# Optimization experiments

Hardware: AMD Instinct MI355X
Metric: run time of the kernel (lower is better)

## Reference

```python
import jax, jax.numpy as jnp
import numpy as np

DIM = 1024
NUM_HEAD = 16
DIM_HEAD = DIM // NUM_HEAD
MAX_SEQ_LEN = 4096
RMS_EPS = 1.1920928955078125e-07  # torch nn.RMSNorm default eps = finfo(fp32).eps
LIN_EPS = 1e-6
PAD_VAL = 1.0
THETA = 10000.0


def rmsnorm(x, g):
    return x * jax.lax.rsqrt(jnp.mean(x * x, axis=-1, keepdims=True) + RMS_EPS) * g


def setup_inputs() -> dict:
    key = jax.random.key(0)
    ks = jax.random.split(key, 20)
    B, L, C, D = 4, 2048, 256, DIM
    s = 1.0 / np.sqrt(D)
    inp = {
        "x": jax.random.normal(ks[0], (B, L, D), jnp.float32),
        "context": jax.random.normal(ks[1], (B, C, D), jnp.float32),
        "attn_mask": jax.random.randint(ks[2], (B, L, L), 0, 2).astype(bool),
        "start_pos": jax.random.randint(ks[3], (B,), 0, MAX_SEQ_LEN - L).astype(jnp.int64),
        "Wqkv": jax.random.normal(ks[4], (D, 3 * D), jnp.float32) * s,
        "bqkv": jax.random.normal(ks[5], (3 * D,), jnp.float32) * 0.01,
        "g_q": jnp.ones((D,), jnp.float32),
        "g_k": jnp.ones((D,), jnp.float32),
        "cWqkv": jax.random.normal(ks[6], (D, 3 * D), jnp.float32) * s,
        "cbqkv": jax.random.normal(ks[7], (3 * D,), jnp.float32) * 0.01,
        "cg_q": jnp.ones((D,), jnp.float32),
        "cg_k": jnp.ones((D,), jnp.float32),
        "Wout": jax.random.normal(ks[8], (D, D), jnp.float32) * s,
        "bout": jax.random.normal(ks[9], (D,), jnp.float32) * 0.01,
        "g_out": jnp.ones((D,), jnp.float32),
        "cWout": jax.random.normal(ks[10], (D, D), jnp.float32) * s,
        "cbout": jax.random.normal(ks[11], (D,), jnp.float32) * 0.01,
        "cg_out": jnp.ones((D,), jnp.float32),
    }
    return inp


def _freqs(pos_indices):
    # pos_indices: (B, L) int
    inv = 1.0 / (THETA ** (jnp.arange(0, DIM_HEAD, 2, dtype=jnp.float32) / DIM_HEAD))  # (DH/2,)
    ang = pos_indices.astype(jnp.float32)[..., None] * inv  # (B, L, DH/2)
    return jnp.cos(ang), jnp.sin(ang)


def _apply_rope(t, cos, sin):
    # t: (B, H, L, DH); cos/sin: (B, L, DH/2) -> broadcast over head
    B, H, L, DH = t.shape
    tr = t.reshape(B, H, L, DH // 2, 2)
    t0, t1 = tr[..., 0], tr[..., 1]
    c = cos[:, None]  # (B,1,L,DH/2)
    s = sin[:, None]
    out = jnp.stack([t0 * c - t1 * s, t0 * s + t1 * c], axis=-1)
    return out.reshape(B, H, L, DH)


def _split_heads(t):
    B, L, D = t.shape
    return t.reshape(B, L, NUM_HEAD, DIM_HEAD).transpose(0, 2, 1, 3)


def _augment_mask(m, C):
    # m: (B, L, L) bool -> (B, L+C, L+C) bool
    B, L, _ = m.shape
    c_to_seq = jnp.broadcast_to(jnp.any(m, axis=1, keepdims=True), (B, C, L))
    seq_to_c = jnp.broadcast_to(jnp.any(m, axis=2, keepdims=True), (B, L, C))
    c_to_c = jnp.ones((B, C, C), bool)
    top = jnp.concatenate([m, seq_to_c], axis=2)
    bot = jnp.concatenate([c_to_seq, c_to_c], axis=2)
    return jnp.concatenate([top, bot], axis=1)


def reference(x, context, attn_mask, start_pos, Wqkv, bqkv, g_q, g_k,
              cWqkv, cbqkv, cg_q, cg_k, Wout, bout, g_out, cWout, cbout, cg_out):
    B, L, D = x.shape
    C = context.shape[1]

    q, k, v = jnp.split(x @ Wqkv + bqkv, 3, axis=-1)
    q = rmsnorm(q, g_q)
    k = rmsnorm(k, g_k)
    q, k, v = _split_heads(q), _split_heads(k), _split_heads(v)  # (B,H,L,DH)

    pos = start_pos[:, None] + jnp.arange(L, dtype=start_pos.dtype)[None]  # (B,L)
    cos, sin = _freqs(pos)
    q = _apply_rope(q, cos, sin)
    k = _apply_rope(k, cos, sin)

    cq, ck, cv = jnp.split(context @ cWqkv + cbqkv, 3, axis=-1)
    cq = rmsnorm(cq, cg_q)
    ck = rmsnorm(ck, cg_k)
    cq, ck, cv = _split_heads(cq), _split_heads(ck), _split_heads(cv)

    q = jnp.concatenate([q, cq], axis=2)  # (B,H,S,DH), S=L+C
    k = jnp.concatenate([k, ck], axis=2)
    v = jnp.concatenate([v, cv], axis=2)

    full_mask = _augment_mask(attn_mask, C)[:, None]  # (B,1,S,S)

    # linear attention: ReLU feature map + padded-value trick
    qf = jax.nn.relu(q)
    kf = jax.nn.relu(k)
    k_mask = full_mask[:, :, 0, :][..., None].astype(kf.dtype)  # (B,1,S,1)
    kf = kf * k_mask
    vpad = jnp.pad(v, ((0, 0), (0, 0), (0, 0), (0, 1)), constant_values=PAD_VAL)  # (B,H,S,DH+1)
    vk = jnp.einsum('bhse,bhsd->bhed', vpad, kf)        # (B,H,DH+1,DH)
    res = jnp.einsum('bhed,bhqd->bhqe', vk, qf)          # (B,H,S,DH+1)
    attn = res[..., :-1] / (res[..., -1:] + LIN_EPS)     # (B,H,S,DH)

    attn = attn.transpose(0, 2, 1, 3).reshape(B, L + C, D)
    x_out = rmsnorm(attn[:, :L] @ Wout + bout, g_out)
    c_out = rmsnorm(attn[:, L:] @ cWout + cbout, cg_out)
    return x_out, c_out
```

## Files before the change

kernel.cpp:

```cpp
#include <hip/hip_runtime.h>

typedef __bf16 bf16;
typedef __bf16 bf16x4 __attribute__((ext_vector_type(4)));
typedef __bf16 bf16x8 __attribute__((ext_vector_type(8)));
typedef float  floatx4 __attribute__((ext_vector_type(4)));

#define L_SEQ   2048
#define C_SEQ   256
#define S_SEQ   2304
#define NBATCH  4
#define NHEAD   16
#define DHEAD   64
#define DMODEL  1024
#define RMS_EPS 1.1920928955078125e-07f
#define LIN_EPS 1e-6f

__device__ __forceinline__ void gload_lds16(const void* g, void* l) {
  __builtin_amdgcn_global_load_lds(
      (const __attribute__((address_space(1))) void*)g,
      (__attribute__((address_space(3))) void*)l, 16, 0, 0);
}

__global__ __launch_bounds__(256) void transpose_f32_bf16(
    const float* __restrict__ src, bf16* __restrict__ dst, int R, int C) {
  __shared__ bf16 tile[32][33];
  int c0 = blockIdx.x * 32, r0 = blockIdx.y * 32;
  int tx = threadIdx.x & 31, ty = threadIdx.x >> 5;
  for (int i = ty; i < 32; i += 8)
    tile[i][tx] = (bf16)src[(size_t)(r0 + i) * C + c0 + tx];
  __syncthreads();
  for (int i = ty; i < 32; i += 8)
    dst[(size_t)(c0 + i) * R + r0 + tx] = tile[tx][i];
}

__global__ __launch_bounds__(256) void convert_bf16(
    const float* __restrict__ src, bf16* __restrict__ dst, size_t n) {
  size_t i = ((size_t)blockIdx.x * 256 + threadIdx.x) * 8;
  if (i >= n) return;
  floatx4 a = *(const floatx4*)(src + i);
  floatx4 b = *(const floatx4*)(src + i + 4);
  bf16x8 o;
#pragma unroll
  for (int j = 0; j < 4; j++) { o[j] = (bf16)a[j]; o[4 + j] = (bf16)b[j]; }
  *(bf16x8*)(dst + i) = o;
}

template <bool SCATTER>
__global__ __launch_bounds__(256) void gemm_bias(
    const bf16* __restrict__ A, const bf16* __restrict__ Bt,
    const float* __restrict__ bias, bf16* __restrict__ C0,
    bf16* __restrict__ qs, bf16* __restrict__ ks, bf16* __restrict__ vs,
    int M, int N, int K, int rpb_shift, int seq_off) {
  __shared__ bf16 As[128 * 32];
  __shared__ bf16 Bs[128 * 32];
  int n0 = blockIdx.x * 128, m0 = blockIdx.y * 128;
  int t = threadIdx.x;
  int lane = t & 63, w = t >> 6;
  int wm = (w & 1) * 64, wn = (w >> 1) * 64;
  int l16 = lane & 15, l4 = lane >> 4;

  int srow = w * 32 + (lane >> 2);
  int scol = (lane & 3) * 8;
  const bf16* Ab = A  + (size_t)(m0 + srow) * K + scol;
  const bf16* Bb = Bt + (size_t)(n0 + srow) * K + scol;

  floatx4 acc[4][4] = {};
  for (int kb = 0; kb < K; kb += 32) {
    __syncthreads();
#pragma unroll
    for (int j = 0; j < 2; j++) {
      gload_lds16(Ab + (size_t)j * 16 * K + kb, (char*)As + (w * 2 + j) * 1024);
      gload_lds16(Bb + (size_t)j * 16 * K + kb, (char*)Bs + (w * 2 + j) * 1024);
    }
    __syncthreads();
    bf16x8 af[4], bfr[4];
#pragma unroll
    for (int i = 0; i < 4; i++) {
      af[i]  = *(const bf16x8*)&As[(wm + i * 16 + l16) * 32 + l4 * 8];
      bfr[i] = *(const bf16x8*)&Bs[(wn + i * 16 + l16) * 32 + l4 * 8];
    }
#pragma unroll
    for (int i = 0; i < 4; i++)
#pragma unroll
      for (int j = 0; j < 4; j++)
        acc[i][j] = __builtin_amdgcn_mfma_f32_16x16x32_bf16(af[i], bfr[j], acc[i][j], 0, 0, 0);
  }
#pragma unroll
  for (int i = 0; i < 4; i++)
#pragma unroll
    for (int j = 0; j < 4; j++) {
      int col = n0 + wn + j * 16 + l16;
      float bval = bias[col];
      if constexpr (SCATTER) {
        int which = col >> 10;
        int h = (col >> 6) & 15;
        int dh = col & 63;
        int rmask = (1 << rpb_shift) - 1;
        if (which == 2) {
          int rw0 = m0 + wm + i * 16 + l4 * 4;
          int b = rw0 >> rpb_shift;
          int s = seq_off + (rw0 & rmask);
          bf16x4 o;
#pragma unroll
          for (int r = 0; r < 4; r++) o[r] = (bf16)(acc[i][j][r] + bval);
          *(bf16x4*)(vs + ((size_t)(b * NHEAD + h) * DHEAD + dh) * S_SEQ + s) = o;
        } else {
          bf16* dst = which == 0 ? qs : ks;
#pragma unroll
          for (int r = 0; r < 4; r++) {
            int rw = m0 + wm + i * 16 + l4 * 4 + r;
            int b = rw >> rpb_shift;
            int s = seq_off + (rw & rmask);
            dst[((size_t)(b * NHEAD + h) * S_SEQ + s) * DHEAD + dh] =
                (bf16)(acc[i][j][r] + bval);
          }
        }
      } else {
#pragma unroll
        for (int r = 0; r < 4; r++) {
          int rw = m0 + wm + i * 16 + l4 * 4 + r;
          C0[(size_t)rw * N + col] = (bf16)(acc[i][j][r] + bval);
        }
      }
    }
}

__global__ __launch_bounds__(256) void anymask_kernel(
    const int* __restrict__ mask, int* __restrict__ anym) {
  int b = blockIdx.x, t = threadIdx.x;
  int a = 0;
  size_t base = (size_t)b * L_SEQ * L_SEQ;
  for (int j = t; j < L_SEQ; j += 256) a |= mask[base + j];
  __shared__ int sh;
  if (t == 0) sh = 0;
  __syncthreads();
  if (a) atomicOr(&sh, 1);
  __syncthreads();
  if (t == 0) anym[b] = sh;
}

__global__ __launch_bounds__(256) void zero_f32(float* __restrict__ p, int n) {
  for (int i = blockIdx.x * 256 + threadIdx.x; i < n; i += gridDim.x * 256)
    p[i] = 0.f;
}

__global__ __launch_bounds__(256) void qkv_post(
    bf16* __restrict__ qs, bf16* __restrict__ ks,
    const int* __restrict__ mask, const int* __restrict__ spos,
    const int* __restrict__ anym,
    const float* __restrict__ g_q, const float* __restrict__ g_k,
    const float* __restrict__ cg_q, const float* __restrict__ cg_k) {
  int g = blockIdx.x, t = threadIdx.x;
  bool is_ctx = g >= NBATCH * L_SEQ;
  int b, s;
  const float *gq, *gk;
  float mval;
  if (!is_ctx) {
    b = g >> 11;
    int l = g & 2047;
    s = l;
    mval = mask[(size_t)b * L_SEQ * L_SEQ + l] ? 1.f : 0.f;
    gq = g_q; gk = g_k;
  } else {
    int gg = g - NBATCH * L_SEQ;
    b = gg >> 8;
    s = L_SEQ + (gg & 255);
    mval = anym[b] ? 1.f : 0.f;
    gq = cg_q; gk = cg_k;
  }
  int d0 = t * 4;
  int h = t >> 4, dh = (t & 15) * 4;
  size_t base = ((size_t)(b * NHEAD + h) * S_SEQ + s) * DHEAD + dh;
  bf16x4 q4 = *(const bf16x4*)(qs + base);
  bf16x4 k4 = *(const bf16x4*)(ks + base);
  float qv[4], kv[4], pq = 0.f, pk = 0.f;
#pragma unroll
  for (int i = 0; i < 4; i++) {
    qv[i] = (float)q4[i]; kv[i] = (float)k4[i];
    pq += qv[i] * qv[i];  pk += kv[i] * kv[i];
  }
  int lane = t & 63, w = t >> 6;
  for (int off = 32; off > 0; off >>= 1) {
    pq += __shfl_down(pq, off, 64);
    pk += __shfl_down(pk, off, 64);
  }
  __shared__ float red[8];
  if (lane == 0) { red[w] = pq; red[4 + w] = pk; }
  __syncthreads();
  float sq = red[0] + red[1] + red[2] + red[3];
  float sk = red[4] + red[5] + red[6] + red[7];
  float scq = rsqrtf(sq * (1.f / DMODEL) + RMS_EPS);
  float sck = rsqrtf(sk * (1.f / DMODEL) + RMS_EPS);
#pragma unroll
  for (int i = 0; i < 4; i++) {
    qv[i] *= scq * gq[d0 + i];
    kv[i] *= sck * gk[d0 + i];
  }
  if (!is_ctx) {
    float p = (float)(spos[b] + s);
#pragma unroll
    for (int pr = 0; pr < 2; pr++) {
      int fi = (dh >> 1) + pr;
      float ang = p * expf((float)fi * -0.28782313662425572f);
      float cc = cosf(ang), ss = sinf(ang);
      float t0 = qv[2 * pr], t1 = qv[2 * pr + 1];
      qv[2 * pr]     = t0 * cc - t1 * ss;
      qv[2 * pr + 1] = t0 * ss + t1 * cc;
      t0 = kv[2 * pr]; t1 = kv[2 * pr + 1];
      kv[2 * pr]     = t0 * cc - t1 * ss;
      kv[2 * pr + 1] = t0 * ss + t1 * cc;
    }
  }
  bf16x4 qo, ko;
#pragma unroll
  for (int i = 0; i < 4; i++) {
    qo[i] = (bf16)fmaxf(qv[i], 0.f);
    ko[i] = (bf16)(fmaxf(kv[i], 0.f) * mval);
  }
  *(bf16x4*)(qs + base) = qo;
  *(bf16x4*)(ks + base) = ko;
}

#define VK_CH   8
#define VK_SPAN (S_SEQ / VK_CH)
__global__ __launch_bounds__(256) void vk_mfma(
    const bf16* __restrict__ vT, const bf16* __restrict__ kf,
    float* __restrict__ vk) {
  __shared__ bf16 Vs[64][40];
  __shared__ bf16 Ks[64][40];
  int bh = blockIdx.x >> 3, chunk = blockIdx.x & 7;
  int t = threadIdx.x, lane = t & 63, w = t >> 6;
  int l16 = lane & 15, l4 = lane >> 4;
  const bf16* vp = vT + (size_t)bh * DHEAD * S_SEQ;
  const bf16* kp = kf + (size_t)bh * S_SEQ * DHEAD;
  int s_begin = chunk * VK_SPAN;
  int ve = t >> 2, vso = (t & 3) * 8;
  int ks_s = t & 31, kd0 = (t >> 5) * 8;
  floatx4 acc[4] = {};
  float dsum[8] = {};
  for (int st = 0; st < VK_SPAN; st += 32) {
    int s0 = s_begin + st;
    bf16x8 vv = *(const bf16x8*)(vp + (size_t)ve * S_SEQ + s0 + vso);
    bf16x8 kv = *(const bf16x8*)(kp + (size_t)(s0 + ks_s) * DHEAD + kd0);
    __syncthreads();
    *(bf16x8*)&Vs[ve][vso] = vv;
#pragma unroll
    for (int j = 0; j < 8; j++) {
      Ks[kd0 + j][ks_s] = kv[j];
      dsum[j] += (float)kv[j];
    }
    __syncthreads();
    bf16x8 af = *(const bf16x8*)&Vs[w * 16 + l16][l4 * 8];
#pragma unroll
    for (int nt = 0; nt < 4; nt++) {
      bf16x8 bfr = *(const bf16x8*)&Ks[nt * 16 + l16][l4 * 8];
      acc[nt] = __builtin_amdgcn_mfma_f32_16x16x32_bf16(af, bfr, acc[nt], 0, 0, 0);
    }
  }
  float* vkbh = vk + (size_t)bh * 65 * 64;
#pragma unroll
  for (int nt = 0; nt < 4; nt++)
#pragma unroll
    for (int r = 0; r < 4; r++)
      atomicAdd(&vkbh[(w * 16 + l4 * 4 + r) * 64 + nt * 16 + l16], acc[nt][r]);
#pragma unroll
  for (int j = 0; j < 8; j++)
#pragma unroll
    for (int off = 16; off > 0; off >>= 1)
      dsum[j] += __shfl_down(dsum[j], off, 32);
  if ((lane & 31) == 0)
#pragma unroll
    for (int j = 0; j < 8; j++)
      atomicAdd(&vkbh[64 * 64 + kd0 + j], dsum[j]);
}

__global__ __launch_bounds__(256) void res_attn(
    const bf16* __restrict__ qf, const float* __restrict__ vk,
    bf16* __restrict__ attn_x, bf16* __restrict__ attn_c) {
  __shared__ bf16 Bs[80][72];
  __shared__ float sden[256];
  int bh = blockIdx.x / 9, mblk = blockIdx.x % 9;
  int b = bh >> 4, h = bh & 15;
  int t = threadIdx.x, lane = t & 63, w = t >> 6;
  const float* vkp = vk + (size_t)bh * 65 * 64;
  for (int i = t; i < 80 * 64; i += 256) {
    int e = i >> 6, d = i & 63;
    Bs[e][d] = (bf16)(e < 65 ? vkp[i] : 0.f);
  }
  __syncthreads();
  int l16 = lane & 15, l4 = lane >> 4;
  const bf16* qbase = qf + (size_t)bh * S_SEQ * DHEAD;
  int q0w = mblk * 256 + w * 64;

  floatx4 acc[4][5] = {};
  bf16x8 af[4][2], bfr[5][2];
#pragma unroll
  for (int mt = 0; mt < 4; mt++) {
    int q = q0w + mt * 16 + l16;
    af[mt][0] = *(const bf16x8*)(qbase + (size_t)q * 64 + l4 * 8);
    af[mt][1] = *(const bf16x8*)(qbase + (size_t)q * 64 + 32 + l4 * 8);
  }
#pragma unroll
  for (int nt = 0; nt < 5; nt++) {
    bfr[nt][0] = *(const bf16x8*)&Bs[nt * 16 + l16][l4 * 8];
    bfr[nt][1] = *(const bf16x8*)&Bs[nt * 16 + l16][32 + l4 * 8];
  }
#pragma unroll
  for (int mt = 0; mt < 4; mt++)
#pragma unroll
    for (int nt = 0; nt < 5; nt++) {
      acc[mt][nt] = __builtin_amdgcn_mfma_f32_16x16x32_bf16(af[mt][0], bfr[nt][0], acc[mt][nt], 0, 0, 0);
      acc[mt][nt] = __builtin_amdgcn_mfma_f32_16x16x32_bf16(af[mt][1], bfr[nt][1], acc[mt][nt], 0, 0, 0);
    }
  if (l16 == 0) {
#pragma unroll
    for (int mt = 0; mt < 4; mt++)
#pragma unroll
      for (int r = 0; r < 4; r++)
        sden[w * 64 + mt * 16 + l4 * 4 + r] = acc[mt][4][r];
  }
  __syncthreads();
#pragma unroll
  for (int mt = 0; mt < 4; mt++)
#pragma unroll
    for (int r = 0; r < 4; r++) {
      float den = sden[w * 64 + mt * 16 + l4 * 4 + r] + LIN_EPS;
      float rden = 1.f / den;
      int q = q0w + mt * 16 + l4 * 4 + r;
#pragma unroll
      for (int nt = 0; nt < 4; nt++) {
        int dcol = nt * 16 + l16;
        float a = acc[mt][nt][r] * rden;
        if (q < L_SEQ)
          attn_x[((size_t)b * L_SEQ + q) * DMODEL + h * DHEAD + dcol] = (bf16)a;
        else
          attn_c[((size_t)b * C_SEQ + (q - L_SEQ)) * DMODEL + h * DHEAD + dcol] = (bf16)a;
      }
    }
}

__global__ __launch_bounds__(256) void final_norm(
    const bf16* __restrict__ y_x, const bf16* __restrict__ y_c,
    const float* __restrict__ g_out, const float* __restrict__ cg_out,
    float* __restrict__ out) {
  int g = blockIdx.x, t = threadIdx.x;
  const bf16* src;
  const float* gv;
  if (g < NBATCH * L_SEQ) {
    src = y_x + (size_t)g * DMODEL; gv = g_out;
  } else {
    int gg = g - NBATCH * L_SEQ;
    src = y_c + (size_t)gg * DMODEL; gv = cg_out;
  }
  float* dst = out + (size_t)g * DMODEL;
  int d0 = t * 4;
  bf16x4 y4 = *(const bf16x4*)(src + d0);
  float yv[4], p = 0.f;
#pragma unroll
  for (int i = 0; i < 4; i++) { yv[i] = (float)y4[i]; p += yv[i] * yv[i]; }
  int lane = t & 63, w = t >> 6;
  for (int off = 32; off > 0; off >>= 1) p += __shfl_down(p, off, 64);
  __shared__ float red[4];
  if (lane == 0) red[w] = p;
  __syncthreads();
  float ssum = red[0] + red[1] + red[2] + red[3];
  float sc = rsqrtf(ssum * (1.f / DMODEL) + RMS_EPS);
  floatx4 o;
#pragma unroll
  for (int i = 0; i < 4; i++) o[i] = yv[i] * sc * gv[d0 + i];
  *(floatx4*)(dst + d0) = o;
}

extern "C" void kernel_launch(void* const* d_in, const int* in_sizes, int n_in,
                              void* d_out, int out_size, void* d_ws, size_t ws_size,
                              hipStream_t stream) {
  const float* x      = (const float*)d_in[0];
  const float* ctx    = (const float*)d_in[1];
  const int*   mask   = (const int*)d_in[2];
  const int*   spos   = (const int*)d_in[3];
  const float* Wqkv   = (const float*)d_in[4];
  const float* bqkv   = (const float*)d_in[5];
  const float* g_q    = (const float*)d_in[6];
  const float* g_k    = (const float*)d_in[7];
  const float* cWqkv  = (const float*)d_in[8];
  const float* cbqkv  = (const float*)d_in[9];
  const float* cg_q   = (const float*)d_in[10];
  const float* cg_k   = (const float*)d_in[11];
  const float* Wout   = (const float*)d_in[12];
  const float* bout   = (const float*)d_in[13];
  const float* g_out  = (const float*)d_in[14];
  const float* cWout  = (const float*)d_in[15];
  const float* cbout  = (const float*)d_in[16];
  const float* cg_out = (const float*)d_in[17];

  char* wsp = (char*)d_ws;
  size_t off = 0;
  auto alloc = [&](size_t bytes) -> void* {
    void* p = wsp + off;
    off += (bytes + 255) & ~(size_t)255;
    return p;
  };
  bf16* WqkvT  = (bf16*)alloc((size_t)3072 * 1024 * 2);
  bf16* cWqkvT = (bf16*)alloc((size_t)3072 * 1024 * 2);
  bf16* WoutT  = (bf16*)alloc((size_t)1024 * 1024 * 2);
  bf16* cWoutT = (bf16*)alloc((size_t)1024 * 1024 * 2);
  bf16* xbf    = (bf16*)alloc((size_t)NBATCH * L_SEQ * DMODEL * 2);
  bf16* cbf    = (bf16*)alloc((size_t)NBATCH * C_SEQ * DMODEL * 2);
  const size_t SLAB = (size_t)NBATCH * NHEAD * S_SEQ * DHEAD;
  bf16* qfs    = (bf16*)alloc(SLAB * 2);
  bf16* kfs    = (bf16*)alloc(SLAB * 2);
  bf16* vfs    = (bf16*)alloc(SLAB * 2);
  float* vkw   = (float*)alloc((size_t)64 * 65 * 64 * 4);
  int* anym    = (int*)alloc(256);
  bf16* attn_x = kfs;
  bf16* attn_c = kfs + (size_t)NBATCH * L_SEQ * DMODEL;
  bf16* y_x    = vfs;
  bf16* y_c    = vfs + (size_t)NBATCH * L_SEQ * DMODEL;

  transpose_f32_bf16<<<dim3(96, 32), 256, 0, stream>>>(Wqkv, WqkvT, 1024, 3072);
  transpose_f32_bf16<<<dim3(96, 32), 256, 0, stream>>>(cWqkv, cWqkvT, 1024, 3072);
  transpose_f32_bf16<<<dim3(32, 32), 256, 0, stream>>>(Wout, WoutT, 1024, 1024);
  transpose_f32_bf16<<<dim3(32, 32), 256, 0, stream>>>(cWout, cWoutT, 1024, 1024);
  convert_bf16<<<4096, 256, 0, stream>>>(x, xbf, (size_t)NBATCH * L_SEQ * DMODEL);
  convert_bf16<<<512, 256, 0, stream>>>(ctx, cbf, (size_t)NBATCH * C_SEQ * DMODEL);

  gemm_bias<true><<<dim3(24, 64), 256, 0, stream>>>(
      xbf, WqkvT, bqkv, nullptr, qfs, kfs, vfs, 8192, 3072, 1024, 11, 0);
  gemm_bias<true><<<dim3(24, 8), 256, 0, stream>>>(
      cbf, cWqkvT, cbqkv, nullptr, qfs, kfs, vfs, 1024, 3072, 1024, 8, L_SEQ);

  anymask_kernel<<<4, 256, 0, stream>>>(mask, anym);
  zero_f32<<<1040, 256, 0, stream>>>(vkw, 64 * 65 * 64);

  qkv_post<<<NBATCH * (L_SEQ + C_SEQ), 256, 0, stream>>>(
      qfs, kfs, mask, spos, anym, g_q, g_k, cg_q, cg_k);

  vk_mfma<<<64 * VK_CH, 256, 0, stream>>>(vfs, kfs, vkw);

  res_attn<<<576, 256, 0, stream>>>(qfs, vkw, attn_x, attn_c);

  gemm_bias<false><<<dim3(8, 64), 256, 0, stream>>>(
      attn_x, WoutT, bout, y_x, nullptr, nullptr, nullptr, 8192, 1024, 1024, 0, 0);
  gemm_bias<false><<<dim3(8, 8), 256, 0, stream>>>(
      attn_c, cWoutT, cbout, y_c, nullptr, nullptr, nullptr, 1024, 1024, 1024, 0, 0);

  final_norm<<<NBATCH * (L_SEQ + C_SEQ), 256, 0, stream>>>(
      y_x, y_c, g_out, cg_out, (float*)d_out);
}
```

Before: 410.8 us.

## Fuse prep kernels, merge paired GEMMs, double-buffer GEMM and vk LDS tiles

The transpose, convert, zero and any-mask kernels are merged into one prep launch, and the x and context GEMMs are each combined into a single grouped launch with XCD-aware workgroup remapping. The GEMM main loop now double-buffers its LDS tiles, issuing the next global-to-LDS load before the MFMAs on the current tile, which removes one barrier per iteration. vk_mfma also double-buffers its shared tiles and prefetches the next chunk into registers. The goals are fewer launches, better tail utilisation and overlap of memory with compute, at the cost of twice the LDS per block.

```diff
diff --git a/kernel.cpp b/kernel.cpp
--- a/kernel.cpp
+++ b/kernel.cpp
@@ -21,10 +21,11 @@
       (__attribute__((address_space(3))) void*)l, 16, 0, 0);
 }
 
-__global__ __launch_bounds__(256) void transpose_f32_bf16(
-    const float* __restrict__ src, bf16* __restrict__ dst, int R, int C) {
-  __shared__ bf16 tile[32][33];
-  int c0 = blockIdx.x * 32, r0 = blockIdx.y * 32;
+__device__ __forceinline__ void transpose_job(
+    const float* __restrict__ src, bf16* __restrict__ dst,
+    int R, int C, int tb, bf16 (*tile)[33]) {
+  int tilesx = C >> 5;
+  int c0 = (tb % tilesx) * 32, r0 = (tb / tilesx) * 32;
   int tx = threadIdx.x & 31, ty = threadIdx.x >> 5;
   for (int i = ty; i < 32; i += 8)
     tile[i][tx] = (bf16)src[(size_t)(r0 + i) * C + c0 + tx];
@@ -33,10 +34,9 @@
     dst[(size_t)(c0 + i) * R + r0 + tx] = tile[tx][i];
 }
 
-__global__ __launch_bounds__(256) void convert_bf16(
-    const float* __restrict__ src, bf16* __restrict__ dst, size_t n) {
-  size_t i = ((size_t)blockIdx.x * 256 + threadIdx.x) * 8;
-  if (i >= n) return;
+__device__ __forceinline__ void convert_job(
+    const float* __restrict__ src, bf16* __restrict__ dst, int tb) {
+  size_t i = ((size_t)tb * 256 + threadIdx.x) * 8;
   floatx4 a = *(const floatx4*)(src + i);
   floatx4 b = *(const floatx4*)(src + i + 4);
   bf16x8 o;
@@ -45,15 +45,78 @@
   *(bf16x8*)(dst + i) = o;
 }
 
+__global__ __launch_bounds__(256) void prep(
+    const float* __restrict__ Wqkv, const float* __restrict__ cWqkv,
+    const float* __restrict__ Wout, const float* __restrict__ cWout,
+    const float* __restrict__ x, const float* __restrict__ ctx,
+    const int* __restrict__ mask,
+    bf16* __restrict__ WqkvT, bf16* __restrict__ cWqkvT,
+    bf16* __restrict__ WoutT, bf16* __restrict__ cWoutT,
+    bf16* __restrict__ xbf, bf16* __restrict__ cbf,
+    float* __restrict__ vkw, int* __restrict__ anym) {
+  __shared__ bf16 tile[32][33];
+  __shared__ int sh;
+  int b = blockIdx.x;
+  if (b < 3072) { transpose_job(Wqkv, WqkvT, 1024, 3072, b, tile); return; }
+  b -= 3072;
+  if (b < 3072) { transpose_job(cWqkv, cWqkvT, 1024, 3072, b, tile); return; }
+  b -= 3072;
+  if (b < 1024) { transpose_job(Wout, WoutT, 1024, 1024, b, tile); return; }
+  b -= 1024;
+  if (b < 1024) { transpose_job(cWout, cWoutT, 1024, 1024, b, tile); return; }
+  b -= 1024;
+  if (b < 4096) { convert_job(x, xbf, b); return; }
+  b -= 4096;
+  if (b < 512) { convert_job(ctx, cbf, b); return; }
+  b -= 512;
+  if (b < 260) {
+    int i = b * 1024 + threadIdx.x * 4;
+    *(floatx4*)(vkw + i) = floatx4{0.f, 0.f, 0.f, 0.f};
+    return;
+  }
+  b -= 260;
+  int a = 0;
+  size_t base = (size_t)b * L_SEQ * L_SEQ;
+  for (int j = threadIdx.x; j < L_SEQ; j += 256) a |= mask[base + j];
+  if (threadIdx.x == 0) sh = 0;
+  __syncthreads();
+  if (a) atomicOr(&sh, 1);
+  __syncthreads();
+  if (threadIdx.x == 0) anym[b] = sh;
+}
+
 template <bool SCATTER>
 __global__ __launch_bounds__(256) void gemm_bias(
-    const bf16* __restrict__ A, const bf16* __restrict__ Bt,
-    const float* __restrict__ bias, bf16* __restrict__ C0,
+    const bf16* __restrict__ A1, const bf16* __restrict__ A2,
+    const bf16* __restrict__ B1t, const bf16* __restrict__ B2t,
+    const float* __restrict__ bias1, const float* __restrict__ bias2,
+    bf16* __restrict__ C1, bf16* __restrict__ C2,
     bf16* __restrict__ qs, bf16* __restrict__ ks, bf16* __restrict__ vs,
-    int M, int N, int K, int rpb_shift, int seq_off) {
-  __shared__ bf16 As[128 * 32];
-  __shared__ bf16 Bs[128 * 32];
-  int n0 = blockIdx.x * 128, m0 = blockIdx.y * 128;
+    int N, int K, int ybound,
+    int rpb1, int soff1, int rpb2, int soff2) {
+  __shared__ bf16 As[2][4096];
+  __shared__ bf16 Bs[2][4096];
+
+  int nwg = gridDim.x * gridDim.y;
+  int wg = blockIdx.y * gridDim.x + blockIdx.x;
+  if ((nwg & 7) == 0) {
+    int cpx = nwg >> 3;
+    wg = (wg & 7) * cpx + (wg >> 3);
+  }
+  int bx = wg % gridDim.x, by = wg / gridDim.x;
+  int n0 = bx * 128;
+  const bf16 *Ap, *Bt;
+  const float* bias;
+  bf16* Cp;
+  int m0, rpb, soff;
+  if (by < ybound) {
+    Ap = A1; Bt = B1t; bias = bias1; Cp = C1;
+    m0 = by * 128; rpb = rpb1; soff = soff1;
+  } else {
+    Ap = A2; Bt = B2t; bias = bias2; Cp = C2;
+    m0 = (by - ybound) * 128; rpb = rpb2; soff = soff2;
+  }
+
   int t = threadIdx.x;
   int lane = t & 63, w = t >> 6;
   int wm = (w & 1) * 64, wn = (w >> 1) * 64;
@@ -61,29 +124,36 @@
 
   int srow = w * 32 + (lane >> 2);
   int scol = (lane & 3) * 8;
-  const bf16* Ab = A  + (size_t)(m0 + srow) * K + scol;
+  const bf16* Ab = Ap + (size_t)(m0 + srow) * K + scol;
   const bf16* Bb = Bt + (size_t)(n0 + srow) * K + scol;
 
+  auto stage = [&](int buf, int kb) {
+#pragma unroll
+    for (int j = 0; j < 2; j++) {
+      gload_lds16(Ab + (size_t)j * 16 * K + kb, (char*)&As[buf][(w * 2 + j) * 512]);
+      gload_lds16(Bb + (size_t)j * 16 * K + kb, (char*)&Bs[buf][(w * 2 + j) * 512]);
+    }
+  };
+
   floatx4 acc[4][4] = {};
+  stage(0, 0);
+  __syncthreads();
+  int cur = 0;
   for (int kb = 0; kb < K; kb += 32) {
-    __syncthreads();
-#pragma unroll
-    for (int j = 0; j < 2; j++) {
-      gload_lds16(Ab + (size_t)j * 16 * K + kb, (char*)As + (w * 2 + j) * 1024);
-      gload_lds16(Bb + (size_t)j * 16 * K + kb, (char*)Bs + (w * 2 + j) * 1024);
-    }
-    __syncthreads();
+    if (kb + 32 < K) stage(cur ^ 1, kb + 32);
     bf16x8 af[4], bfr[4];
 #pragma unroll
     for (int i = 0; i < 4; i++) {
-      af[i]  = *(const bf16x8*)&As[(wm + i * 16 + l16) * 32 + l4 * 8];
-      bfr[i] = *(const bf16x8*)&Bs[(wn + i * 16 + l16) * 32 + l4 * 8];
+      af[i]  = *(const bf16x8*)&As[cur][(wm + i * 16 + l16) * 32 + l4 * 8];
+      bfr[i] = *(const bf16x8*)&Bs[cur][(wn + i * 16 + l16) * 32 + l4 * 8];
     }
 #pragma unroll
     for (int i = 0; i < 4; i++)
 #pragma unroll
       for (int j = 0; j < 4; j++)
         acc[i][j] = __builtin_amdgcn_mfma_f32_16x16x32_bf16(af[i], bfr[j], acc[i][j], 0, 0, 0);
+    __syncthreads();
+    cur ^= 1;
   }
 #pragma unroll
   for (int i = 0; i < 4; i++)
@@ -95,11 +165,11 @@
         int which = col >> 10;
         int h = (col >> 6) & 15;
         int dh = col & 63;
-        int rmask = (1 << rpb_shift) - 1;
+        int rmask = (1 << rpb) - 1;
         if (which == 2) {
           int rw0 = m0 + wm + i * 16 + l4 * 4;
-          int b = rw0 >> rpb_shift;
-          int s = seq_off + (rw0 & rmask);
+          int b = rw0 >> rpb;
+          int s = soff + (rw0 & rmask);
           bf16x4 o;
 #pragma unroll
           for (int r = 0; r < 4; r++) o[r] = (bf16)(acc[i][j][r] + bval);
@@ -109,8 +179,8 @@
 #pragma unroll
           for (int r = 0; r < 4; r++) {
             int rw = m0 + wm + i * 16 + l4 * 4 + r;
-            int b = rw >> rpb_shift;
-            int s = seq_off + (rw & rmask);
+            int b = rw >> rpb;
+            int s = soff + (rw & rmask);
             dst[((size_t)(b * NHEAD + h) * S_SEQ + s) * DHEAD + dh] =
                 (bf16)(acc[i][j][r] + bval);
           }
@@ -119,29 +189,10 @@
 #pragma unroll
         for (int r = 0; r < 4; r++) {
           int rw = m0 + wm + i * 16 + l4 * 4 + r;
-          C0[(size_t)rw * N + col] = (bf16)(acc[i][j][r] + bval);
+          Cp[(size_t)rw * N + col] = (bf16)(acc[i][j][r] + bval);
         }
       }
     }
-}
-
-__global__ __launch_bounds__(256) void anymask_kernel(
-    const int* __restrict__ mask, int* __restrict__ anym) {
-  int b = blockIdx.x, t = threadIdx.x;
-  int a = 0;
-  size_t base = (size_t)b * L_SEQ * L_SEQ;
-  for (int j = t; j < L_SEQ; j += 256) a |= mask[base + j];
-  __shared__ int sh;
-  if (t == 0) sh = 0;
-  __syncthreads();
-  if (a) atomicOr(&sh, 1);
-  __syncthreads();
-  if (t == 0) anym[b] = sh;
-}
-
-__global__ __launch_bounds__(256) void zero_f32(float* __restrict__ p, int n) {
-  for (int i = blockIdx.x * 256 + threadIdx.x; i < n; i += gridDim.x * 256)
-    p[i] = 0.f;
 }
 
 __global__ __launch_bounds__(256) void qkv_post(
@@ -226,8 +277,8 @@
 __global__ __launch_bounds__(256) void vk_mfma(
     const bf16* __restrict__ vT, const bf16* __restrict__ kf,
     float* __restrict__ vk) {
-  __shared__ bf16 Vs[64][40];
-  __shared__ bf16 Ks[64][40];
+  __shared__ bf16 Vs[2][64][40];
+  __shared__ bf16 Ks[2][64][40];
   int bh = blockIdx.x >> 3, chunk = blockIdx.x & 7;
   int t = threadIdx.x, lane = t & 63, w = t >> 6;
   int l16 = lane & 15, l4 = lane >> 4;
@@ -238,22 +289,26 @@
   int ks_s = t & 31, kd0 = (t >> 5) * 8;
   floatx4 acc[4] = {};
   float dsum[8] = {};
+  bf16x8 vv = *(const bf16x8*)(vp + (size_t)ve * S_SEQ + s_begin + vso);
+  bf16x8 kv = *(const bf16x8*)(kp + (size_t)(s_begin + ks_s) * DHEAD + kd0);
   for (int st = 0; st < VK_SPAN; st += 32) {
-    int s0 = s_begin + st;
-    bf16x8 vv = *(const bf16x8*)(vp + (size_t)ve * S_SEQ + s0 + vso);
-    bf16x8 kv = *(const bf16x8*)(kp + (size_t)(s0 + ks_s) * DHEAD + kd0);
+    int cur = (st >> 5) & 1;
+    *(bf16x8*)&Vs[cur][ve][vso] = vv;
+#pragma unroll
+    for (int j = 0; j < 8; j++) {
+      Ks[cur][kd0 + j][ks_s] = kv[j];
+      dsum[j] += (float)kv[j];
+    }
+    if (st + 32 < VK_SPAN) {
+      int s0 = s_begin + st + 32;
+      vv = *(const bf16x8*)(vp + (size_t)ve * S_SEQ + s0 + vso);
+      kv = *(const bf16x8*)(kp + (size_t)(s0 + ks_s) * DHEAD + kd0);
+    }
     __syncthreads();
-    *(bf16x8*)&Vs[ve][vso] = vv;
-#pragma unroll
-    for (int j = 0; j < 8; j++) {
-      Ks[kd0 + j][ks_s] = kv[j];
-      dsum[j] += (float)kv[j];
-    }
-    __syncthreads();
-    bf16x8 af = *(const bf16x8*)&Vs[w * 16 + l16][l4 * 8];
+    bf16x8 af = *(const bf16x8*)&Vs[cur][w * 16 + l16][l4 * 8];
 #pragma unroll
     for (int nt = 0; nt < 4; nt++) {
-      bf16x8 bfr = *(const bf16x8*)&Ks[nt * 16 + l16][l4 * 8];
+      bf16x8 bfr = *(const bf16x8*)&Ks[cur][nt * 16 + l16][l4 * 8];
       acc[nt] = __builtin_amdgcn_mfma_f32_16x16x32_bf16(af, bfr, acc[nt], 0, 0, 0);
     }
   }
@@ -417,20 +472,13 @@
   bf16* y_x    = vfs;
   bf16* y_c    = vfs + (size_t)NBATCH * L_SEQ * DMODEL;
 
-  transpose_f32_bf16<<<dim3(96, 32), 256, 0, stream>>>(Wqkv, WqkvT, 1024, 3072);
-  transpose_f32_bf16<<<dim3(96, 32), 256, 0, stream>>>(cWqkv, cWqkvT, 1024, 3072);
-  transpose_f32_bf16<<<dim3(32, 32), 256, 0, stream>>>(Wout, WoutT, 1024, 1024);
-  transpose_f32_bf16<<<dim3(32, 32), 256, 0, stream>>>(cWout, cWoutT, 1024, 1024);
-  convert_bf16<<<4096, 256, 0, stream>>>(x, xbf, (size_t)NBATCH * L_SEQ * DMODEL);
-  convert_bf16<<<512, 256, 0, stream>>>(ctx, cbf, (size_t)NBATCH * C_SEQ * DMODEL);
-
-  gemm_bias<true><<<dim3(24, 64), 256, 0, stream>>>(
-      xbf, WqkvT, bqkv, nullptr, qfs, kfs, vfs, 8192, 3072, 1024, 11, 0);
-  gemm_bias<true><<<dim3(24, 8), 256, 0, stream>>>(
-      cbf, cWqkvT, cbqkv, nullptr, qfs, kfs, vfs, 1024, 3072, 1024, 8, L_SEQ);
-
-  anymask_kernel<<<4, 256, 0, stream>>>(mask, anym);
-  zero_f32<<<1040, 256, 0, stream>>>(vkw, 64 * 65 * 64);
+  prep<<<13064, 256, 0, stream>>>(Wqkv, cWqkv, Wout, cWout, x, ctx, mask,
+                                  WqkvT, cWqkvT, WoutT, cWoutT, xbf, cbf,
+                                  vkw, anym);
+
+  gemm_bias<true><<<dim3(24, 72), 256, 0, stream>>>(
+      xbf, cbf, WqkvT, cWqkvT, bqkv, cbqkv, nullptr, nullptr,
+      qfs, kfs, vfs, 3072, 1024, 64, 11, 0, 8, L_SEQ);
 
   qkv_post<<<NBATCH * (L_SEQ + C_SEQ), 256, 0, stream>>>(
       qfs, kfs, mask, spos, anym, g_q, g_k, cg_q, cg_k);
@@ -439,10 +487,9 @@
 
   res_attn<<<576, 256, 0, stream>>>(qfs, vkw, attn_x, attn_c);
 
-  gemm_bias<false><<<dim3(8, 64), 256, 0, stream>>>(
-      attn_x, WoutT, bout, y_x, nullptr, nullptr, nullptr, 8192, 1024, 1024, 0, 0);
-  gemm_bias<false><<<dim3(8, 8), 256, 0, stream>>>(
-      attn_c, cWoutT, cbout, y_c, nullptr, nullptr, nullptr, 1024, 1024, 1024, 0, 0);
+  gemm_bias<false><<<dim3(8, 72), 256, 0, stream>>>(
+      attn_x, attn_c, WoutT, cWoutT, bout, cbout, y_x, y_c,
+      nullptr, nullptr, nullptr, 1024, 1024, 64, 0, 0, 0, 0);
 
   final_norm<<<NBATCH * (L_SEQ + C_SEQ), 256, 0, stream>>>(
       y_x, y_c, g_out, cg_out, (float*)d_out);
```

Measured after the change: 356.6 us. 1.15x faster.
